# Kernel tuning notes

Hardware: AMD Instinct MI355X
Metric: run time of the kernel (lower is better)

The kernel has to match this reference:

```python
import jax, jax.numpy as jnp
import numpy as np

N, C, NDIM = 32768, 128, 64
ALPHA, BETA = 1.0, 0.0


def setup_inputs() -> dict:
    key = jax.random.key(0)
    kx, kp, ka = jax.random.split(key, 3)
    eye = jnp.eye(NDIM, dtype=jnp.float32)
    # SPD inputs: X = M M^T / n + eps*I  (well-conditioned, distinct eigvals)
    Mx = jax.random.normal(kx, (N, NDIM, NDIM), dtype=jnp.float32)
    X = Mx @ jnp.swapaxes(Mx, -1, -2) / NDIM + 1e-3 * eye
    # SPD class prototypes P: small perturbation of identity (source inits to I)
    Mp = 0.1 * jax.random.normal(kp, (C, NDIM, NDIM), dtype=jnp.float32)
    P = Mp @ jnp.swapaxes(Mp, -1, -2) / NDIM + eye
    # A: init_matrix_uniform with fan_in = n^2, factor 6
    bound = float(np.sqrt(6.0 / (NDIM * NDIM)))
    A = jax.random.uniform(ka, (C, NDIM, NDIM), dtype=jnp.float32,
                           minval=-bound, maxval=bound)
    return {"X": X, "P": P, "A": A}


def _symmetrize_by_tril(A):
    # strict lower + its transpose + diagonal, as in symmetrize_by_tril
    L = jnp.tril(A, -1)
    d = jnp.diagonal(A, axis1=-2, axis2=-1)  # (..., n)
    eye = jnp.eye(A.shape[-1], dtype=A.dtype)
    return L + jnp.swapaxes(L, -1, -2) + eye * d[..., None, :]


def _logm(M):
    # batched SPD matrix logarithm via eigendecomposition
    w, v = jnp.linalg.eigh(M)
    return (v * jnp.log(w)[..., None, :]) @ jnp.swapaxes(v, -1, -2)


def reference(X, P, A):
    """Log-Euclidean RMLR: logit[n,c] = <Log X_n - Log P_c, A_c>^(alpha,beta)
    where <V,W> = alpha*tr(V W) + beta*tr(V)*tr(W), A_c symmetric."""
    A_sym = _symmetrize_by_tril(A)            # (C, n, n)
    logX = _logm(X)                           # (N, n, n)
    logP = _logm(P)                           # (C, n, n)
    # tr((logX - logP) A_sym) without materializing (N,C,n,n)
    lin = (jnp.einsum('nij,cij->nc', logX, A_sym)
           - jnp.einsum('cij,cij->c', logP, A_sym)[None, :])
    out = ALPHA * lin
    if BETA != 0.0:
        trX = jnp.trace(logX, axis1=-2, axis2=-1)   # (N,)
        trP = jnp.trace(logP, axis1=-2, axis2=-1)   # (C,)
        trA = jnp.trace(A_sym, axis1=-2, axis2=-1)  # (C,)
        out = out + BETA * (trX[:, None] - trP[None, :]) * trA[None, :]
    return out  # (N, C)
```

## Files before the change

kernel.cpp:

```cpp
#include <hip/hip_runtime.h>
#include <math.h>

#define N_X 32768
#define N_P 128
#define ND 64
#define MAT (ND*ND)
#define NWAVE 4
#define BISECT_ITERS 26

typedef float v2f __attribute__((ext_vector_type(2)));

#if __has_builtin(__builtin_elementwise_fma)
__device__ __forceinline__ v2f vfma(v2f a, v2f b, v2f c) {
    return __builtin_elementwise_fma(a, b, c);
}
#else
__device__ __forceinline__ v2f vfma(v2f a, v2f b, v2f c) {
    return v2f{fmaf(a.x, b.x, c.x), fmaf(a.y, b.y, c.y)};
}
#endif

__device__ __forceinline__ float wsum(float t) {
    #pragma unroll
    for (int m = 1; m < 64; m <<= 1) t += __shfl_xor(t, m);
    return t;
}

__device__ __forceinline__ float frcp(float x) {
    return __builtin_amdgcn_rcpf(x);
}

__device__ __forceinline__ float guard_piv(float p) {
    return (fabsf(p) < 1e-22f) ? -1e-22f : p;
}

__device__ __forceinline__ void lds_fence() {
    asm volatile("s_waitcnt lgkmcnt(0)" ::: "memory");
}


__global__ __launch_bounds__(256) void symmetrize_kernel(float* __restrict__ A) {
    const int idx = blockIdx.x * 256 + threadIdx.x;
    const int r   = (idx >> 6) & 63;
    const int col = idx & 63;
    if (col > r) A[idx] = A[(idx & ~4095) | (col << 6) | r];
}

__global__ __launch_bounds__(256) void tridiag_kernel(float* __restrict__ X,
                                                      float* __restrict__ P,
                                                      float* __restrict__ coefs) {
    __shared__ __align__(16) float scrb[NWAVE][64];
    __shared__ __align__(16) float vrowb[NWAVE][64];
    __shared__ __align__(16) float urowb[NWAVE][64];
    __shared__ __align__(8)  v2f  DEb[NWAVE][64];
    const int wid  = threadIdx.x >> 6;
    const int lane = threadIdx.x & 63;
    const int b    = blockIdx.x * NWAVE + wid;
    float* M = (b < N_X) ? (X + (size_t)b * MAT)
                         : (P + (size_t)(b - N_X) * MAT);
    float* scr  = scrb[wid];
    float* vrow = vrowb[wid];
    float* urow = urowb[wid];
    v2f*   DE   = DEb[wid];

    float wcol[64];
    float dg = 0.f;
    #pragma unroll
    for (int i = 0; i < 64; ++i) {
        wcol[i] = M[i * ND + lane];
        if (i == lane) dg = wcol[i];
    }
    float ereg = 0.f;

    #pragma unroll 1
    for (int k = 0; k < 62; ++k) {
        if (lane == k) {
            #pragma unroll
            for (int j = 0; j < 16; ++j)
                *(float4*)(&scr[4 * j]) =
                    make_float4(wcol[4*j], wcol[4*j+1], wcol[4*j+2], wcol[4*j+3]);
        }
        __syncthreads();

        const float xj = scr[lane];
        const float x0 = scr[k + 1];
        const float nx2 = wsum((lane > k) ? xj * xj : 0.f);
        const float normx = sqrtf(nx2);
        const float alpha = -copysignf(normx, x0);
        const float vn2   = 2.f * (nx2 - alpha * x0);
        const bool  ok    = (nx2 > 1e-40f);
        const float rvn   = ok ? rsqrtf(vn2) : 0.f;
        float vj = 0.f;
        if (lane == k + 1)      vj = (x0 - alpha) * rvn;
        else if (lane > k)      vj = xj * rvn;
        vrow[lane] = vj;
        if (lane == k) ereg = alpha;
        __syncthreads();
        M[k * ND + lane] = vj;

        v2f vv[32];
        {
            const float4* vp = (const float4*)(&vrow[0]);
            #pragma unroll
            for (int j = 0; j < 16; ++j) {
                const float4 q = vp[j];
                vv[2*j]   = v2f{q.x, q.y};
                vv[2*j+1] = v2f{q.z, q.w};
            }
        }
        v2f acc = {0.f, 0.f};
        #pragma unroll
        for (int j = 0; j < 32; ++j)
            acc = vfma(v2f{wcol[2*j], wcol[2*j+1]}, vv[j], acc);
        const float wj = 2.f * (acc.x + acc.y);
        const float K  = wsum(vj * wj);
        const float uj = wj - K * vj;
        urow[lane] = uj;
        __syncthreads();

        {
            const float4* up = (const float4*)(&urow[0]);
            const v2f vjv = {vj, vj}, ujv = {uj, uj};
            #pragma unroll
            for (int j = 0; j < 16; ++j) {
                const float4 q = up[j];
                v2f u0 = {q.x, q.y}, u1 = {q.z, q.w};
                v2f w0 = {wcol[4*j],   wcol[4*j+1]};
                v2f w1 = {wcol[4*j+2], wcol[4*j+3]};
                w0 = vfma(-vv[2*j],   ujv, vfma(-u0, vjv, w0));
                w1 = vfma(-vv[2*j+1], ujv, vfma(-u1, vjv, w1));
                wcol[4*j]   = w0.x; wcol[4*j+1] = w0.y;
                wcol[4*j+2] = w1.x; wcol[4*j+3] = w1.y;
            }
        }
        dg -= 2.f * uj * vj;
    }

    if (lane == 62) ereg = wcol[63];
    DE[lane] = v2f{dg, ereg};
    __syncthreads();

    float glo = 1e30f, ghi = -1e30f;
    {
        float eprev = 0.f;
        #pragma unroll
        for (int i = 0; i < 64; ++i) {
            const v2f t = DE[i];
            const float e = (i < 63) ? fabsf(t.y) : 0.f;
            const float r = e + eprev;
            glo = fminf(glo, t.x - r);
            ghi = fmaxf(ghi, t.x + r);
            eprev = e;
        }
    }
    float lo = glo, hi = ghi;
    #pragma unroll 1
    for (int it = 0; it < BISECT_ITERS; ++it) {
        const float mid = 0.5f * (lo + hi);
        int cnt = 0;
        float p = 1.f, eprev = 0.f;
        #pragma unroll
        for (int i = 0; i < 64; ++i) {
            const v2f t = DE[i];
            const float num = eprev * eprev;
            p = (t.x - mid) - num * frcp(p);
            p = guard_piv(p);
            cnt += (p < 0.f) ? 1 : 0;
            eprev = t.y;
        }
        if (cnt <= lane) lo = mid; else hi = mid;
    }
    const float lam = 0.5f * (lo + hi);

    M[62 * ND + lane] = dg;
    M[63 * ND + lane] = ereg;
    coefs[(size_t)b * ND + lane] = lam;
}

__global__ __launch_bounds__(256) void eigvec_kernel(float* __restrict__ X,
                                                     float* __restrict__ P,
                                                     float* __restrict__ coefs) {
    __shared__ __align__(8)  v2f  DEb[NWAVE][64];
    __shared__ __align__(16) float vrowb[NWAVE][64];
    const int wid  = threadIdx.x >> 6;
    const int lane = threadIdx.x & 63;
    const int b    = blockIdx.x * NWAVE + wid;
    float* M = (b < N_X) ? (X + (size_t)b * MAT)
                         : (P + (size_t)(b - N_X) * MAT);
    v2f*   DE   = DEb[wid];
    float* vrow = vrowb[wid];

    const float dg   = M[62 * ND + lane];
    const float ereg = M[63 * ND + lane];
    const float lam  = coefs[(size_t)b * ND + lane];
    DE[lane] = v2f{dg, ereg};
    __syncthreads();

    float rden[64], y[64];
    {
        float eprev;
        {
            const v2f t0 = DE[0];
            rden[0] = frcp(guard_piv(t0.x - lam));
            eprev = t0.y;
            y[0] = 0.7548f;
        }
        #pragma unroll
        for (int i = 1; i < 64; ++i) {
            const v2f ti = DE[i];
            const float m = eprev * rden[i-1];
            rden[i] = frcp(guard_piv((ti.x - lam) - m * eprev));
            const float bi = (float)(((unsigned)(i * 2654435761u)
                               ^ (unsigned)((lane + 1) * 40503u)) & 0xFFFFu)
                               * 3.0517578e-05f - 0.5f;
            y[i] = bi - m * y[i-1];
            eprev = ti.y;
        }
        y[63] *= rden[63];
        #pragma unroll
        for (int i = 62; i >= 0; --i)
            y[i] = (y[i] - DE[i].y * y[i+1]) * rden[i];

        float n2 = 0.f;
        #pragma unroll
        for (int i = 0; i < 64; ++i) n2 = fmaf(y[i], y[i], n2);
        const float rn = rsqrtf(fmaxf(n2, 1e-30f));
        y[0] *= rn;
        eprev = DE[0].y;
        #pragma unroll
        for (int i = 1; i < 64; ++i) {
            const float m = eprev * rden[i-1];
            y[i] = y[i] * rn - m * y[i-1];
            eprev = DE[i].y;
        }
        y[63] *= rden[63];
        #pragma unroll
        for (int i = 62; i >= 0; --i)
            y[i] = (y[i] - DE[i].y * y[i+1]) * rden[i];
        n2 = 0.f;
        #pragma unroll
        for (int i = 0; i < 64; ++i) n2 = fmaf(y[i], y[i], n2);
        const float rn2 = rsqrtf(fmaxf(n2, 1e-30f));
        #pragma unroll
        for (int i = 0; i < 64; ++i) y[i] *= rn2;
    }

    {
        const float lamprev = __shfl(lam, lane - 1);
        const bool doGS = (lane > 0) && ((lam - lamprev) < 1e-3f * fabsf(lam));
        float dot = 0.f;
        #pragma unroll
        for (int i = 0; i < 64; ++i)
            dot = fmaf(y[i], __shfl(y[i], lane - 1), dot);
        const float s = doGS ? dot : 0.f;
        float n2 = 0.f;
        #pragma unroll
        for (int i = 0; i < 64; ++i) {
            const float ypi = __shfl(y[i], lane - 1);
            y[i] = fmaf(-s, ypi, y[i]);
            n2 = fmaf(y[i], y[i], n2);
        }
        const float rn = rsqrtf(fmaxf(n2, 1e-30f));
        #pragma unroll
        for (int i = 0; i < 64; ++i) y[i] *= rn;
    }

    #pragma unroll 1
    for (int k = 61; k >= 0; --k) {
        const float gv = M[k * ND + lane];
        vrow[lane] = gv;
        lds_fence();
        const float4* vp = (const float4*)(&vrow[0]);
        v2f acc = {0.f, 0.f};
        #pragma unroll
        for (int j = 0; j < 16; ++j) {
            const float4 q = vp[j];
            acc = vfma(v2f{y[4*j],   y[4*j+1]}, v2f{q.x, q.y}, acc);
            acc = vfma(v2f{y[4*j+2], y[4*j+3]}, v2f{q.z, q.w}, acc);
        }
        const float s2 = 2.f * (acc.x + acc.y);
        #pragma unroll
        for (int j = 0; j < 16; ++j) {
            const float4 q = vp[j];
            y[4*j+0] = fmaf(-s2, q.x, y[4*j+0]);
            y[4*j+1] = fmaf(-s2, q.y, y[4*j+1]);
            y[4*j+2] = fmaf(-s2, q.z, y[4*j+2]);
            y[4*j+3] = fmaf(-s2, q.w, y[4*j+3]);
        }
    }

    #pragma unroll
    for (int i = 0; i < 64; ++i) M[i * ND + lane] = y[i];
    coefs[(size_t)b * ND + lane] = logf(fmaxf(lam, 1e-12f));
}

__global__ __launch_bounds__(256, 4) void recompose_kernel(float* __restrict__ X,
                                                           float* __restrict__ P,
                                                           const float* __restrict__ coefs) {
    __shared__ __align__(16) float WR[ND][68];
    __shared__ float Cf[ND];
    const int b = blockIdx.x;
    float* M = (b < N_X) ? (X + (size_t)b * MAT)
                         : (P + (size_t)(b - N_X) * MAT);
    const int tid = threadIdx.x;

    {
        const int r = tid >> 2, q = (tid & 3) * 16;
        const float4 v0 = *(const float4*)(&M[r * ND + q + 0]);
        const float4 v1 = *(const float4*)(&M[r * ND + q + 4]);
        const float4 v2 = *(const float4*)(&M[r * ND + q + 8]);
        const float4 v3 = *(const float4*)(&M[r * ND + q + 12]);
        WR[q+ 0][r]=v0.x; WR[q+ 1][r]=v0.y; WR[q+ 2][r]=v0.z; WR[q+ 3][r]=v0.w;
        WR[q+ 4][r]=v1.x; WR[q+ 5][r]=v1.y; WR[q+ 6][r]=v1.z; WR[q+ 7][r]=v1.w;
        WR[q+ 8][r]=v2.x; WR[q+ 9][r]=v2.y; WR[q+10][r]=v2.z; WR[q+11][r]=v2.w;
        WR[q+12][r]=v3.x; WR[q+13][r]=v3.y; WR[q+14][r]=v3.z; WR[q+15][r]=v3.w;
    }
    if (tid < ND) Cf[tid] = coefs[(size_t)b * ND + tid];
    __syncthreads();

    const int tx = tid & 15, ty = tid >> 4;

    v2f a00={0,0},a01={0,0},a10={0,0},a11={0,0},
        a20={0,0},a21={0,0},a30={0,0},a31={0,0};

    #pragma unroll 4
    for (int k = 0; k < ND; ++k) {
        const v2f* row = (const v2f*)(&WR[k][0]);
        const float sk = Cf[k];
        const v2f skv = {sk, sk};
        const v2f aA = row[ty*2], aB = row[ty*2 + 1];
        const v2f b0 = row[tx*2] * skv, b1 = row[tx*2 + 1] * skv;
        const v2f ax0 = {aA.x, aA.x}, ax1 = {aA.y, aA.y};
        const v2f ax2 = {aB.x, aB.x}, ax3 = {aB.y, aB.y};
        a00 = vfma(ax0, b0, a00);  a01 = vfma(ax0, b1, a01);
        a10 = vfma(ax1, b0, a10);  a11 = vfma(ax1, b1, a11);
        a20 = vfma(ax2, b0, a20);  a21 = vfma(ax2, b1, a21);
        a30 = vfma(ax3, b0, a30);  a31 = vfma(ax3, b1, a31);
    }

    const int i0 = ty * 4, j0 = tx * 4;
    *(float4*)(&M[(size_t)(i0+0)*ND + j0]) = make_float4(a00.x,a00.y,a01.x,a01.y);
    *(float4*)(&M[(size_t)(i0+1)*ND + j0]) = make_float4(a10.x,a10.y,a11.x,a11.y);
    *(float4*)(&M[(size_t)(i0+2)*ND + j0]) = make_float4(a20.x,a20.y,a21.x,a21.y);
    *(float4*)(&M[(size_t)(i0+3)*ND + j0]) = make_float4(a30.x,a30.y,a31.x,a31.y);
}

__global__ __launch_bounds__(64) void off_kernel(const float* __restrict__ LP,
                                                 const float* __restrict__ AS,
                                                 float* __restrict__ off) {
    const int c = blockIdx.x, lane = threadIdx.x;
    const float* lp = LP + (size_t)c * MAT;
    const float* as = AS + (size_t)c * MAT;
    float t = 0.f;
    #pragma unroll 8
    for (int i = 0; i < ND; ++i)
        t = fmaf(lp[i * ND + lane], as[i * ND + lane], t);
    #pragma unroll
    for (int m = 32; m >= 1; m >>= 1) t += __shfl_xor(t, m);
    if (lane == 0) off[c] = t;
}

__global__ __launch_bounds__(256) void logits_kernel(const float* __restrict__ LX,
                                                     const float* __restrict__ AS,
                                                     const float* __restrict__ off,
                                                     float* __restrict__ out) {
    __shared__ __align__(16) float LXs[32][132];
    __shared__ __align__(16) float ASs[32][132];
    const int tid = threadIdx.x;
    const int tx = tid & 15, ty = tid >> 4;
    const int nbase = blockIdx.x * 128;

    float offv[8];
    #pragma unroll
    for (int j = 0; j < 8; ++j) offv[j] = off[tx * 8 + j];

    float acc[8][8];
    #pragma unroll
    for (int i = 0; i < 8; ++i)
        #pragma unroll
        for (int j = 0; j < 8; ++j) acc[i][j] = 0.f;

    #pragma unroll 1
    for (int kc = 0; kc < MAT; kc += 32) {
        #pragma unroll
        for (int u = 0; u < 4; ++u) {
            const int f  = u * 256 + tid;
            const int r  = f >> 3;
            const int c4 = (f & 7) * 4;
            const float4 v = *(const float4*)(&LX[(size_t)(nbase + r) * MAT + kc + c4]);
            LXs[c4+0][r] = v.x; LXs[c4+1][r] = v.y; LXs[c4+2][r] = v.z; LXs[c4+3][r] = v.w;
            const float4 g = *(const float4*)(&AS[(size_t)r * MAT + kc + c4]);
            ASs[c4+0][r] = g.x; ASs[c4+1][r] = g.y; ASs[c4+2][r] = g.z; ASs[c4+3][r] = g.w;
        }
        __syncthreads();
        #pragma unroll 4
        for (int kk = 0; kk < 32; ++kk) {
            const float4 a0 = *(const float4*)(&LXs[kk][ty * 8]);
            const float4 a1 = *(const float4*)(&LXs[kk][ty * 8 + 4]);
            const float4 b0 = *(const float4*)(&ASs[kk][tx * 8]);
            const float4 b1 = *(const float4*)(&ASs[kk][tx * 8 + 4]);
            const float av[8] = {a0.x,a0.y,a0.z,a0.w,a1.x,a1.y,a1.z,a1.w};
            const float bv[8] = {b0.x,b0.y,b0.z,b0.w,b1.x,b1.y,b1.z,b1.w};
            #pragma unroll
            for (int i = 0; i < 8; ++i)
                #pragma unroll
                for (int j = 0; j < 8; ++j)
                    acc[i][j] = fmaf(av[i], bv[j], acc[i][j]);
        }
        __syncthreads();
    }

    #pragma unroll
    for (int i = 0; i < 8; ++i) {
        const int n = nbase + ty * 8 + i;
        const float4 o0 = make_float4(acc[i][0]-offv[0], acc[i][1]-offv[1],
                                      acc[i][2]-offv[2], acc[i][3]-offv[3]);
        const float4 o1 = make_float4(acc[i][4]-offv[4], acc[i][5]-offv[5],
                                      acc[i][6]-offv[6], acc[i][7]-offv[7]);
        *(float4*)(&out[(size_t)n * 128 + tx * 8])     = o0;
        *(float4*)(&out[(size_t)n * 128 + tx * 8 + 4]) = o1;
    }
}

extern "C" void kernel_launch(void* const* d_in, const int* in_sizes, int n_in,
                              void* d_out, int out_size, void* d_ws, size_t ws_size,
                              hipStream_t stream) {
    float* X   = (float*)d_in[0];
    float* P   = (float*)d_in[1];
    float* A   = (float*)d_in[2];
    float* out = (float*)d_out;
    float* off = (float*)d_ws;
    float* coefs = (float*)d_out;

    hipLaunchKernelGGL(symmetrize_kernel, dim3((N_P * MAT) / 256),   dim3(256), 0, stream, A);
    hipLaunchKernelGGL(tridiag_kernel,    dim3((N_X + N_P) / NWAVE), dim3(256), 0, stream, X, P, coefs);
    hipLaunchKernelGGL(eigvec_kernel,     dim3((N_X + N_P) / NWAVE), dim3(256), 0, stream, X, P, coefs);
    hipLaunchKernelGGL(recompose_kernel,  dim3(N_X + N_P),           dim3(256), 0, stream, X, P, coefs);
    hipLaunchKernelGGL(off_kernel,        dim3(N_P),                 dim3(64),  0, stream, P, A, off);
    hipLaunchKernelGGL(logits_kernel,     dim3(N_X / 128),           dim3(256), 0, stream, X, A, off, out);
}
```

Measured before the change: 5.609 ms.

## Run tridiagonalization as one wave per block with wave-level LDS fences

The tridiagonal reduction kernel now launches one 64-thread block per matrix instead of four independent waves per 256-thread block. Its block-wide barriers become an LDS waitcnt plus a scheduling barrier, so one wave no longer stalls on the other three. In the back-transformation loop, the global load of the next Householder vector is issued one iteration early to hide its latency. This relies on a single wavefront running in lockstep for LDS visibility, and it quadruples the number of blocks launched.

Result: faster. 4.592 ms (-18.1%).

```diff
diff --git a/kernel.cpp b/kernel.cpp
--- a/kernel.cpp
+++ b/kernel.cpp
@@ -34,8 +34,9 @@
     return (fabsf(p) < 1e-22f) ? -1e-22f : p;
 }
 
-__device__ __forceinline__ void lds_fence() {
+__device__ __forceinline__ void wave_sync() {
     asm volatile("s_waitcnt lgkmcnt(0)" ::: "memory");
+    __builtin_amdgcn_sched_barrier(0);
 }
 
 
@@ -46,22 +47,17 @@
     if (col > r) A[idx] = A[(idx & ~4095) | (col << 6) | r];
 }
 
-__global__ __launch_bounds__(256) void tridiag_kernel(float* __restrict__ X,
-                                                      float* __restrict__ P,
-                                                      float* __restrict__ coefs) {
-    __shared__ __align__(16) float scrb[NWAVE][64];
-    __shared__ __align__(16) float vrowb[NWAVE][64];
-    __shared__ __align__(16) float urowb[NWAVE][64];
-    __shared__ __align__(8)  v2f  DEb[NWAVE][64];
-    const int wid  = threadIdx.x >> 6;
-    const int lane = threadIdx.x & 63;
-    const int b    = blockIdx.x * NWAVE + wid;
+__global__ __launch_bounds__(64) void tridiag_kernel(float* __restrict__ X,
+                                                     float* __restrict__ P,
+                                                     float* __restrict__ coefs) {
+    __shared__ __align__(16) float scr[64];
+    __shared__ __align__(16) float vrow[64];
+    __shared__ __align__(16) float urow[64];
+    __shared__ __align__(8)  v2f  DE[64];
+    const int lane = threadIdx.x;
+    const int b    = blockIdx.x;
     float* M = (b < N_X) ? (X + (size_t)b * MAT)
                          : (P + (size_t)(b - N_X) * MAT);
-    float* scr  = scrb[wid];
-    float* vrow = vrowb[wid];
-    float* urow = urowb[wid];
-    v2f*   DE   = DEb[wid];
 
     float wcol[64];
     float dg = 0.f;
@@ -80,7 +76,7 @@
                 *(float4*)(&scr[4 * j]) =
                     make_float4(wcol[4*j], wcol[4*j+1], wcol[4*j+2], wcol[4*j+3]);
         }
-        __syncthreads();
+        wave_sync();
 
         const float xj = scr[lane];
         const float x0 = scr[k + 1];
@@ -94,9 +90,9 @@
         if (lane == k + 1)      vj = (x0 - alpha) * rvn;
         else if (lane > k)      vj = xj * rvn;
         vrow[lane] = vj;
+        M[k * ND + lane] = vj;
         if (lane == k) ereg = alpha;
-        __syncthreads();
-        M[k * ND + lane] = vj;
+        wave_sync();
 
         v2f vv[32];
         {
@@ -116,7 +112,7 @@
         const float K  = wsum(vj * wj);
         const float uj = wj - K * vj;
         urow[lane] = uj;
-        __syncthreads();
+        wave_sync();
 
         {
             const float4* up = (const float4*)(&urow[0]);
@@ -138,7 +134,7 @@
 
     if (lane == 62) ereg = wcol[63];
     DE[lane] = v2f{dg, ereg};
-    __syncthreads();
+    wave_sync();
 
     float glo = 1e30f, ghi = -1e30f;
     {
@@ -265,11 +261,13 @@
         for (int i = 0; i < 64; ++i) y[i] *= rn;
     }
 
+    float gv = M[61 * ND + lane];
     #pragma unroll 1
     for (int k = 61; k >= 0; --k) {
-        const float gv = M[k * ND + lane];
         vrow[lane] = gv;
-        lds_fence();
+        asm volatile("s_waitcnt lgkmcnt(0)" ::: "memory");
+        if (k > 0) gv = M[(k - 1) * ND + lane];
+        __builtin_amdgcn_sched_barrier(0);
         const float4* vp = (const float4*)(&vrow[0]);
         v2f acc = {0.f, 0.f};
         #pragma unroll
@@ -433,7 +431,7 @@
     float* coefs = (float*)d_out;
 
     hipLaunchKernelGGL(symmetrize_kernel, dim3((N_P * MAT) / 256),   dim3(256), 0, stream, A);
-    hipLaunchKernelGGL(tridiag_kernel,    dim3((N_X + N_P) / NWAVE), dim3(256), 0, stream, X, P, coefs);
+    hipLaunchKernelGGL(tridiag_kernel,    dim3(N_X + N_P),           dim3(64),  0, stream, X, P, coefs);
     hipLaunchKernelGGL(eigvec_kernel,     dim3((N_X + N_P) / NWAVE), dim3(256), 0, stream, X, P, coefs);
     hipLaunchKernelGGL(recompose_kernel,  dim3(N_X + N_P),           dim3(256), 0, stream, X, P, coefs);
     hipLaunchKernelGGL(off_kernel,        dim3(N_P),                 dim3(64),  0, stream, P, A, off);
```
